# Kernel tuning notes

Hardware: AMD Instinct MI355X
Metric: run time of the kernel (lower is better)

## Reference

```python
import jax, jax.numpy as jnp
import numpy as np

# dims
B, T, D, H, DFF, NTYPE = 8, 1024, 512, 8, 1024, 341
HD = D // H                    # 64 head dim
NUM_AXES = 1
DPR = D // H // (NUM_AXES + 1) # 32 dims rotated per axis
EPS = 1e-5
THETA = 10000.0


def layernorm(x, g, b):
    m = jnp.mean(x, axis=-1, keepdims=True)
    v = jnp.mean((x - m) ** 2, axis=-1, keepdims=True)
    return (x - m) * jax.lax.rsqrt(v + EPS) * g + b


def swiglu(x):
    a, gate = jnp.split(x, 2, axis=-1)
    return jax.nn.silu(gate) * a


def apply_rope(x, pos):
    # x: [B,H,T,DPR], pos: [B,T] float positions (possibly non-integer / scrambled order)
    inv_freq = 1.0 / (THETA ** (jnp.arange(0, DPR, 2, dtype=jnp.float32) / DPR))  # [DPR/2]
    freqs = pos[:, None, :, None] * inv_freq          # [B,1,T,DPR/2]
    cos = jnp.repeat(jnp.cos(freqs), 2, axis=-1)      # each freq repeated twice -> [B,1,T,DPR]
    sin = jnp.repeat(jnp.sin(freqs), 2, axis=-1)
    x1 = x[..., 0::2]
    x2 = x[..., 1::2]
    rot = jnp.stack([-x2, x1], axis=-1).reshape(x.shape)  # rotate_half, interleaved pairs
    return x * cos + rot * sin


def setup_inputs() -> dict:
    key = jax.random.key(0)
    ks = jax.random.split(key, 16)
    s = lambda d: 1.0 / np.sqrt(d)
    return {
        "x_type": jax.random.randint(ks[0], (B, T + 1), 0, NTYPE),
        "x_value": jax.random.normal(ks[1], (B, T, D), dtype=jnp.float32),
        "seq_order": jax.random.uniform(ks[2], (B, T + 1), dtype=jnp.float32) * T,
        "W_attn": jax.random.normal(ks[3], (D, 3 * D), dtype=jnp.float32) * s(D),
        "type_emb": jax.random.normal(ks[4], (NTYPE, 2 * D), dtype=jnp.float32) * 0.02,
        "ln1_g": jnp.ones((D,), jnp.float32),
        "ln1_b": jnp.zeros((D,), jnp.float32),
        "ln2_g": jnp.ones((D,), jnp.float32),
        "ln2_b": jnp.zeros((D,), jnp.float32),
        "W1": jax.random.normal(ks[5], (D, 2 * DFF), dtype=jnp.float32) * s(D),
        "b1": jnp.zeros((2 * DFF,), jnp.float32),
        "W2": jax.random.normal(ks[6], (DFF, D), dtype=jnp.float32) * s(DFF),
        "b2": jnp.zeros((D,), jnp.float32),
    }


def reference(x_type, x_value, seq_order, W_attn, type_emb, ln1_g, ln1_b, ln2_g, ln2_b, W1, b1, W2, b2):
    # --- attention sublayer ---
    h = layernorm(x_value, ln1_g, ln1_b)                  # [B,T,D]
    qkv = h @ W_attn                                      # [B,T,3D]
    q, k, v = jnp.split(qkv, 3, axis=-1)
    emb = type_emb[x_type]                                # [B,T+1,2D]
    q_embed, k_embed = jnp.split(emb, 2, axis=-1)
    q = q + q_embed[:, :-1]
    k = k + k_embed[:, 1:]
    # [B,H,T,HD]
    to_heads = lambda t: t.reshape(B, T, H, HD).transpose(0, 2, 1, 3)
    q, k, v = to_heads(q), to_heads(k), to_heads(v)
    # rotate first DPR dims with (shifted) seq_order; remaining dims untouched
    q = jnp.concatenate([apply_rope(q[..., :DPR], seq_order[:, :-1]), q[..., DPR:]], axis=-1)
    k = jnp.concatenate([apply_rope(k[..., :DPR], seq_order[:, 1:]), k[..., DPR:]], axis=-1)
    # causal SDPA
    scores = jnp.einsum("bhqd,bhkd->bhqk", q, k) / jnp.sqrt(jnp.float32(HD))
    causal = jnp.tril(jnp.ones((T, T), dtype=bool))
    scores = jnp.where(causal, scores, -jnp.inf)
    attn = jax.nn.softmax(scores, axis=-1)
    out = jnp.einsum("bhqk,bhkd->bhqd", attn, v)          # [B,H,T,HD]
    out = out.transpose(0, 2, 1, 3).reshape(B, T, D)
    x = x_value + out
    # --- SwiGLU FFN sublayer ---
    h2 = layernorm(x, ln2_g, ln2_b)
    ff = swiglu(h2 @ W1 + b1) @ W2 + b2
    return x + ff
```

## Files before the change

kernel.cpp:

```cpp
#include <hip/hip_runtime.h>
#include <stdint.h>
#include <math.h>

typedef unsigned short u16;
typedef unsigned int u32;
typedef __attribute__((ext_vector_type(8))) short bf16x8;
typedef __attribute__((ext_vector_type(4))) float f32x4;
typedef __attribute__((ext_vector_type(2))) float f32x2;
typedef __attribute__((ext_vector_type(2))) u16 u16x2;
typedef __attribute__((ext_vector_type(8))) u16 u16x8;
typedef __attribute__((ext_vector_type(2))) u32 u32x2;

#define B_ 8
#define T_ 1024
#define D_ 512
#define H_ 8
#define TP1 1025
#define QSCALE 0.1803368801111204f

__device__ __forceinline__ u16 f2b(float f) {
  union { float f; u32 u; } v; v.f = f;
  return (u16)((v.u + 0x7fffu + ((v.u >> 16) & 1u)) >> 16);
}
__device__ __forceinline__ void gld16(const void* g, void* l) {
  __builtin_amdgcn_global_load_lds((const __attribute__((address_space(1))) u32*)g,
                                   (__attribute__((address_space(3))) u32*)l, 16, 0, 0);
}
__device__ __forceinline__ f32x4 mfma16(bf16x8 a, bf16x8 b, f32x4 c) {
  return __builtin_amdgcn_mfma_f32_16x16x32_bf16(a, b, c, 0, 0, 0);
}
__device__ __forceinline__ u32 cvtpk(float lo, float hi) {
  u32 r;
  asm("v_cvt_pk_bf16_f32 %0, %1, %2" : "=v"(r) : "v"(lo), "v"(hi));
  return r;
}
union U8 { u32 u[4]; bf16x8 v; };

#define WAITV(N) asm volatile("s_waitcnt vmcnt(" #N ")" ::: "memory")

__global__ __launch_bounds__(256) void prep_kernel(const float* __restrict__ W_attn,
    const float* __restrict__ W1, const float* __restrict__ W2,
    const float* __restrict__ seq,
    u16* __restrict__ WtA, u16* __restrict__ W1i, u16* __restrict__ W2t,
    float* __restrict__ cq, float* __restrict__ sq_,
    float* __restrict__ ck, float* __restrict__ sk) {
  int bid = blockIdx.x, tid = threadIdx.x;
  if (bid >= 576) {
    int i = (bid - 576) * 256 + tid;
    int p = i & 15, bt = i >> 4, b = bt >> 10, t = bt & 1023;
    float inv = expf(-(float)p * 0.5756462732485115f);
    float aq = seq[b * TP1 + t] * inv;
    float ak = seq[b * TP1 + t + 1] * inv;
    cq[i] = cosf(aq); sq_[i] = sinf(aq);
    ck[i] = cosf(ak); sk[i] = sinf(ak);
    return;
  }
  __shared__ u16 lt[64][65];
  const float* src; u16* dst; int ld, Kd, k0, r0; bool ilv = false;
  if (bid < 192) {
    src = W_attn; dst = WtA; ld = 1536; Kd = 512;
    k0 = (bid & 7) * 64; r0 = (bid >> 3) * 64;
  } else if (bid < 448) {
    int t = bid - 192;
    src = W1; dst = W1i; ld = 2048; Kd = 512; ilv = true;
    k0 = (t & 7) * 64; r0 = (t >> 3) * 64;
  } else {
    int t = bid - 448;
    src = W2; dst = W2t; ld = 512; Kd = 1024;
    k0 = (t & 15) * 64; r0 = (t >> 4) * 64;
  }
  int nl = tid & 63;
  int scol, rloc;
  if (ilv) {
    if (nl < 32) { scol = (r0 >> 1) + nl;          rloc = ((nl >> 4) << 5) + (nl & 15); }
    else         { scol = 1024 + (r0 >> 1) + (nl - 32); rloc = (((nl - 32) >> 4) << 5) + 16 + (nl & 15); }
  } else { scol = r0 + nl; rloc = nl; }
  #pragma unroll
  for (int it = 0; it < 16; it++) {
    int kl = (tid >> 6) * 16 + it;
    lt[rloc][kl] = f2b(src[(size_t)(k0 + kl) * ld + scol]);
  }
  __syncthreads();
  #pragma unroll
  for (int it = 0; it < 16; it++) {
    int rl = (tid >> 6) * 16 + it;
    dst[(size_t)(r0 + rl) * Kd + k0 + nl] = lt[rl][nl];
  }
}

__global__ __launch_bounds__(256) void ln_kernel(const float* __restrict__ x,
    const float* __restrict__ g, const float* __restrict__ bta, u16* __restrict__ out) {
  int row = blockIdx.x * 4 + (threadIdx.x >> 6);
  int lane = threadIdx.x & 63;
  const float* xr = x + (size_t)row * D_ + lane * 8;
  f32x4 v0 = *(const f32x4*)xr;
  f32x4 v1 = *(const f32x4*)(xr + 4);
  float s = 0.f, sq = 0.f;
  #pragma unroll
  for (int j = 0; j < 4; j++) { s += v0[j] + v1[j]; sq += v0[j] * v0[j] + v1[j] * v1[j]; }
  #pragma unroll
  for (int m = 1; m < 64; m <<= 1) { s += __shfl_xor(s, m); sq += __shfl_xor(sq, m); }
  float mean = s * (1.f / D_);
  float var = sq * (1.f / D_) - mean * mean;
  float rstd = rsqrtf(var + 1e-5f);
  f32x4 g0 = *(const f32x4*)(g + lane * 8);
  f32x4 g1 = *(const f32x4*)(g + lane * 8 + 4);
  f32x4 b0 = *(const f32x4*)(bta + lane * 8);
  f32x4 b1 = *(const f32x4*)(bta + lane * 8 + 4);
  u16x8 o;
  #pragma unroll
  for (int j = 0; j < 4; j++) {
    o[j]     = f2b((v0[j] - mean) * rstd * g0[j] + b0[j]);
    o[4 + j] = f2b((v1[j] - mean) * rstd * g1[j] + b1[j]);
  }
  *(u16x8*)(out + (size_t)row * D_ + lane * 8) = o;
}

__global__ __launch_bounds__(256) void gemm_qkv(const u16* __restrict__ A,
    const u16* __restrict__ Bt,
    const int* __restrict__ x_type, const float* __restrict__ type_emb,
    const float* __restrict__ rqc, const float* __restrict__ rqs,
    const float* __restrict__ rkc, const float* __restrict__ rks,
    u16* __restrict__ qT, u16* __restrict__ kT, u16* __restrict__ vT) {
  __shared__ u16 lA[3][4096];
  __shared__ u16 lB[3][4096];
  const int K = 512, NK = 16;
  const int tid = threadIdx.x, lane = tid & 63, w = tid >> 6;
  const int wm = w >> 1, wn = w & 1;
  int swz = (blockIdx.x & 7) * 96 + (blockIdx.x >> 3);
  int byy = swz / 12, bxx = swz - byy * 12;
  const size_t bm = (size_t)byy * 128;
  const size_t bn = (size_t)bxx * 128;

  const int r0 = tid >> 2;
  const int cs = ((tid & 3) ^ ((r0 >> 1) & 3)) * 8;
  const u16* a0 = A + (bm + r0) * K + cs;
  const u16* a1 = A + (bm + 64 + r0) * K + cs;
  const u16* b0 = Bt + (bn + r0) * K + cs;
  const u16* b1p = Bt + (bn + 64 + r0) * K + cs;

  int aoff[4], boff[4];
  #pragma unroll
  for (int i = 0; i < 4; i++) {
    int ra = wm * 64 + i * 16 + (lane & 15);
    aoff[i] = ra * 64 + (((lane >> 4) ^ ((ra >> 1) & 3)) * 16);
    int rb = wn * 64 + i * 16 + (lane & 15);
    boff[i] = rb * 64 + (((lane >> 4) ^ ((rb >> 1) & 3)) * 16);
  }

  auto stage = [&](int j, int buf) {
    char* ad = (char*)lA + buf * 8192 + w * 1024;
    char* bd = (char*)lB + buf * 8192 + w * 1024;
    gld16(a0 + j * 32, ad);
    gld16(a1 + j * 32, ad + 4096);
    gld16(b0 + j * 32, bd);
    gld16(b1p + j * 32, bd + 4096);
  };
  f32x4 acc[4][4] = {};
  auto compute = [&](int buf) {
    const char* lAc = (const char*)lA + buf * 8192;
    const char* lBc = (const char*)lB + buf * 8192;
    bf16x8 af[4], bf[4];
    #pragma unroll
    for (int i = 0; i < 4; i++) af[i] = *(const bf16x8*)(lAc + aoff[i]);
    #pragma unroll
    for (int n = 0; n < 4; n++) bf[n] = *(const bf16x8*)(lBc + boff[n]);
    __builtin_amdgcn_s_setprio(1);
    #pragma unroll
    for (int i = 0; i < 4; i++)
      #pragma unroll
      for (int n = 0; n < 4; n++)
        acc[i][n] = mfma16(af[i], bf[n], acc[i][n]);
    __builtin_amdgcn_s_setprio(0);
  };

  stage(0, 0);
  stage(1, 1);
  int cur = 0;
  for (int j = 0; j < NK - 1; j++) {
    WAITV(4);
    __builtin_amdgcn_s_barrier();
    if (j + 2 < NK) { int nb = cur + 2; if (nb >= 3) nb -= 3; stage(j + 2, nb); }
    compute(cur);
    cur = (cur + 1 == 3) ? 0 : cur + 1;
  }
  WAITV(0);
  __builtin_amdgcn_s_barrier();
  compute(cur);

  const int region = (int)(bn >> 9);
  #pragma unroll
  for (int i = 0; i < 4; i++) {
    #pragma unroll
    for (int jj = 0; jj < 4; jj++) {
      int row = (int)bm + wm * 64 + i * 16 + (lane >> 4) * 4 + jj;
      int b = row >> 10, t = row & 1023;
      if (region == 0) {
        int ty = x_type[b * TP1 + t];
        #pragma unroll
        for (int n = 0; n < 4; n++) {
          int cloc = (int)bn + wn * 64 + n * 16 + (lane & 15);
          int h = cloc >> 6, hd = cloc & 63;
          float v = acc[i][n][jj] + type_emb[(size_t)ty * 1024 + cloc];
          float vp = __shfl_xor(v, 1);
          if (hd < 32) {
            int p = hd >> 1;
            float c = rqc[row * 16 + p], s = rqs[row * 16 + p];
            v = (hd & 1) ? (v * c + vp * s) : (v * c - vp * s);
          }
          qT[((size_t)(b * 8 + h) * T_ + t) * 64 + hd] = f2b(v * QSCALE);
        }
      } else if (region == 1) {
        int ty = x_type[b * TP1 + t + 1];
        #pragma unroll
        for (int n = 0; n < 4; n++) {
          int cloc = (int)bn - 512 + wn * 64 + n * 16 + (lane & 15);
          int h = cloc >> 6, hd = cloc & 63;
          float v = acc[i][n][jj] + type_emb[(size_t)ty * 1024 + 512 + cloc];
          float vp = __shfl_xor(v, 1);
          if (hd < 32) {
            int p = hd >> 1;
            float c = rkc[row * 16 + p], s = rks[row * 16 + p];
            v = (hd & 1) ? (v * c + vp * s) : (v * c - vp * s);
          }
          kT[((size_t)(b * 8 + h) * T_ + t) * 64 + hd] = f2b(v);
        }
      } else {
        #pragma unroll
        for (int n = 0; n < 4; n++) {
          int cloc = (int)bn - 1024 + wn * 64 + n * 16 + (lane & 15);
          int h = cloc >> 6, hd = cloc & 63;
          vT[((size_t)(b * 8 + h) * 64 + hd) * T_ + t] = f2b(acc[i][n][jj]);
        }
      }
    }
  }
}

__global__ __launch_bounds__(256) void gemm_ff1(const u16* __restrict__ A,
    const u16* __restrict__ Bt, const float* __restrict__ b1,
    u16* __restrict__ outp) {
  __shared__ u16 lA[3][4096];
  __shared__ u16 lB[3][4096];
  const int K = 512, NK = 16;
  const int tid = threadIdx.x, lane = tid & 63, w = tid >> 6;
  const int wm = w >> 1, wn = w & 1;
  int swz = (blockIdx.x & 7) * 128 + (blockIdx.x >> 3);
  int byy = swz >> 4, bxx = swz & 15;
  const size_t bm = (size_t)byy * 128;
  const size_t bn = (size_t)bxx * 128;

  const int r0 = tid >> 2;
  const int cs = ((tid & 3) ^ ((r0 >> 1) & 3)) * 8;
  const u16* a0 = A + (bm + r0) * K + cs;
  const u16* a1 = A + (bm + 64 + r0) * K + cs;
  const u16* b0 = Bt + (bn + r0) * K + cs;
  const u16* b1p = Bt + (bn + 64 + r0) * K + cs;

  int aoff[4], boff[4];
  #pragma unroll
  for (int i = 0; i < 4; i++) {
    int ra = wm * 64 + i * 16 + (lane & 15);
    aoff[i] = ra * 64 + (((lane >> 4) ^ ((ra >> 1) & 3)) * 16);
    int rb = wn * 64 + i * 16 + (lane & 15);
    boff[i] = rb * 64 + (((lane >> 4) ^ ((rb >> 1) & 3)) * 16);
  }

  auto stage = [&](int j, int buf) {
    char* ad = (char*)lA + buf * 8192 + w * 1024;
    char* bd = (char*)lB + buf * 8192 + w * 1024;
    gld16(a0 + j * 32, ad);
    gld16(a1 + j * 32, ad + 4096);
    gld16(b0 + j * 32, bd);
    gld16(b1p + j * 32, bd + 4096);
  };
  f32x4 acc[4][4] = {};
  auto compute = [&](int buf) {
    const char* lAc = (const char*)lA + buf * 8192;
    const char* lBc = (const char*)lB + buf * 8192;
    bf16x8 af[4], bf[4];
    #pragma unroll
    for (int i = 0; i < 4; i++) af[i] = *(const bf16x8*)(lAc + aoff[i]);
    #pragma unroll
    for (int n = 0; n < 4; n++) bf[n] = *(const bf16x8*)(lBc + boff[n]);
    __builtin_amdgcn_s_setprio(1);
    #pragma unroll
    for (int i = 0; i < 4; i++)
      #pragma unroll
      for (int n = 0; n < 4; n++)
        acc[i][n] = mfma16(af[i], bf[n], acc[i][n]);
    __builtin_amdgcn_s_setprio(0);
  };

  stage(0, 0);
  stage(1, 1);
  int cur = 0;
  for (int j = 0; j < NK - 1; j++) {
    WAITV(4);
    __builtin_amdgcn_s_barrier();
    if (j + 2 < NK) { int nb = cur + 2; if (nb >= 3) nb -= 3; stage(j + 2, nb); }
    compute(cur);
    cur = (cur + 1 == 3) ? 0 : cur + 1;
  }
  WAITV(0);
  __builtin_amdgcn_s_barrier();
  compute(cur);

  #pragma unroll
  for (int np = 0; np < 2; np++) {
    int c = ((int)bn >> 1) + wn * 32 + np * 16 + (lane & 15);
    float bav = b1[c], bgv = b1[1024 + c];
    #pragma unroll
    for (int i = 0; i < 4; i++) {
      #pragma unroll
      for (int jj = 0; jj < 4; jj++) {
        int row = (int)bm + wm * 64 + i * 16 + (lane >> 4) * 4 + jj;
        float av = acc[i][2 * np][jj] + bav;
        float gv = acc[i][2 * np + 1][jj] + bgv;
        float sg = gv / (1.f + expf(-gv));
        outp[(size_t)row * 1024 + c] = f2b(sg * av);
      }
    }
  }
}

__global__ __launch_bounds__(512) void gemm_ff2(const u16* __restrict__ A,
    const u16* __restrict__ Bt, const float* __restrict__ bias,
    float* __restrict__ C) {
  __shared__ u16 lA[3][4096];
  __shared__ u16 lB[3][4096];
  const int K = 1024, N = 512, NK = 32;
  const int tid = threadIdx.x, lane = tid & 63, w = tid >> 6;
  const int wm = w >> 2, wn = w & 3;
  int swz = (blockIdx.x & 7) * 32 + (blockIdx.x >> 3);
  int byy = swz >> 2, bxx = swz & 3;
  const size_t bm = (size_t)byy * 128;
  const size_t bn = (size_t)bxx * 128;

  const int r0 = tid >> 2;
  const int cs = ((tid & 3) ^ ((r0 >> 1) & 3)) * 8;
  const u16* a0 = A + (bm + r0) * K + cs;
  const u16* b0 = Bt + (bn + r0) * K + cs;

  int aoff[4], boff[2];
  #pragma unroll
  for (int i = 0; i < 4; i++) {
    int ra = wm * 64 + i * 16 + (lane & 15);
    aoff[i] = ra * 64 + (((lane >> 4) ^ ((ra >> 1) & 3)) * 16);
  }
  #pragma unroll
  for (int n = 0; n < 2; n++) {
    int rb = wn * 32 + n * 16 + (lane & 15);
    boff[n] = rb * 64 + (((lane >> 4) ^ ((rb >> 1) & 3)) * 16);
  }

  auto stage = [&](int j, int buf) {
    gld16(a0 + j * 32, (char*)lA + buf * 8192 + w * 1024);
    gld16(b0 + j * 32, (char*)lB + buf * 8192 + w * 1024);
  };
  f32x4 acc[4][2] = {};
  auto compute = [&](int buf) {
    const char* lAc = (const char*)lA + buf * 8192;
    const char* lBc = (const char*)lB + buf * 8192;
    bf16x8 af[4], bf[2];
    #pragma unroll
    for (int i = 0; i < 4; i++) af[i] = *(const bf16x8*)(lAc + aoff[i]);
    #pragma unroll
    for (int n = 0; n < 2; n++) bf[n] = *(const bf16x8*)(lBc + boff[n]);
    __builtin_amdgcn_s_setprio(1);
    #pragma unroll
    for (int i = 0; i < 4; i++)
      #pragma unroll
      for (int n = 0; n < 2; n++)
        acc[i][n] = mfma16(af[i], bf[n], acc[i][n]);
    __builtin_amdgcn_s_setprio(0);
  };

  stage(0, 0);
  stage(1, 1);
  int cur = 0;
  for (int j = 0; j < NK - 1; j++) {
    WAITV(2);
    __builtin_amdgcn_s_barrier();
    if (j + 2 < NK) { int nb = cur + 2; if (nb >= 3) nb -= 3; stage(j + 2, nb); }
    compute(cur);
    cur = (cur + 1 == 3) ? 0 : cur + 1;
  }
  WAITV(0);
  __builtin_amdgcn_s_barrier();
  compute(cur);

  #pragma unroll
  for (int i = 0; i < 4; i++) {
    size_t mrow = bm + wm * 64 + i * 16 + (lane >> 4) * 4;
    #pragma unroll
    for (int n = 0; n < 2; n++) {
      size_t col = bn + wn * 32 + n * 16 + (lane & 15);
      float bv = bias[col];
      #pragma unroll
      for (int jj = 0; jj < 4; jj++) {
        size_t idx = (mrow + jj) * (size_t)N + col;
        C[idx] = acc[i][n][jj] + bv + C[idx];
      }
    }
  }
}

__global__ __launch_bounds__(512, 4) void attn_kernel(const u16* __restrict__ qT,
    const u16* __restrict__ kT, const u16* __restrict__ vT,
    const float* __restrict__ xv, float* __restrict__ X) {
  int s0 = (blockIdx.x & 7) * 64 + (blockIdx.x >> 3);
  const int xcd = blockIdx.x & 7;
  (void)xcd;
  const int bh = ((blockIdx.x & 7) << 3) + (s0 & 7);
  const int qp = 7 - ((s0 >> 3) & 7);
  const int b = bh >> 3, h = bh & 7;
  const int tid = threadIdx.x, lane = tid & 63, w = tid >> 6;
  const int q = lane & 15, g = lane >> 4;
  __shared__ u16 lK[2][8192];
  __shared__ u16 lV[2][8192];

  const int qrow0 = qp * 128 + w * 16;
  bf16x8 qf[2];
  {
    const u16* qp_ = qT + ((size_t)bh * T_ + qrow0 + q) * 64 + g * 8;
    qf[0] = *(const bf16x8*)qp_;
    qf[1] = *(const bf16x8*)(qp_ + 32);
  }
  f32x4 acc[4] = {};
  float mr = -1e30f, lr = 0.f;

  const int sr = tid >> 3;
  const int scs = ((tid & 7) ^ (sr & 7)) * 8;
  const u16* kb = kT + ((size_t)bh * T_ + sr) * 64 + scs;
  const u16* vb = vT + ((size_t)bh * 64 + sr) * T_ + scs;

  auto stage = [&](int j, int buf) {
    char* kd = (char*)lK + buf * 16384 + w * 1024;
    char* vd = (char*)lV + buf * 16384 + w * 1024;
    gld16(kb + (size_t)j * 8192, kd);
    gld16(kb + (size_t)j * 8192 + 4096, kd + 8192);
    gld16(vb + j * 128, vd);
    gld16(vb + j * 128 + 64, vd + 8192);
  };

  const int jmax = qp + 1;
  stage(0, 0);
  __syncthreads();
  int cur = 0;
  for (int j = 0; j < jmax; j++) {
    if (j + 1 < jmax) stage(j + 1, cur ^ 1);
    const char* lKc = (const char*)lK + cur * 16384;
    const char* lVc = (const char*)lV + cur * 16384;

    f32x4 s[8] = {};
    __builtin_amdgcn_s_setprio(1);
    #pragma unroll
    for (int ka = 0; ka < 2; ka++) {
      #pragma unroll
      for (int n = 0; n < 8; n++) {
        bf16x8 kf = *(const bf16x8*)(lKc + (n >> 2) * 8192 + ((n & 3) * 16 + q) * 128 +
                                     (((ka * 4 + g) ^ (q & 7)) * 16));
        s[n] = mfma16(kf, qf[ka], s[n]);
      }
    }
    __builtin_amdgcn_s_setprio(0);
    if (j == jmax - 1) {
      int qrow = w * 16 + q;
      #pragma unroll
      for (int n = 0; n < 8; n++)
        #pragma unroll
        for (int i = 0; i < 4; i++)
          if (n * 16 + g * 4 + i > qrow) s[n][i] = -1e30f;
    }
    float mt = -1e30f;
    #pragma unroll
    for (int n = 0; n < 8; n++)
      mt = fmaxf(mt, fmaxf(fmaxf(s[n][0], s[n][1]), fmaxf(s[n][2], s[n][3])));
    mt = fmaxf(mt, __shfl_xor(mt, 16));
    mt = fmaxf(mt, __shfl_xor(mt, 32));
    if (__any(mt > mr + 8.f)) {
      float mnew = fmaxf(mr, mt);
      float sc = exp2f(mr - mnew);
      mr = mnew;
      lr *= sc;
      #pragma unroll
      for (int t = 0; t < 4; t++) acc[t] *= sc;
    }
    float ps = 0.f;
    U8 pa[4];
    #pragma unroll
    for (int kt = 0; kt < 4; kt++) {
      float p0[4], p1[4];
      #pragma unroll
      for (int i = 0; i < 4; i++) {
        p0[i] = exp2f(s[2 * kt][i] - mr);
        p1[i] = exp2f(s[2 * kt + 1][i] - mr);
        ps += p0[i] + p1[i];
      }
      pa[kt].u[0] = cvtpk(p0[0], p0[1]);
      pa[kt].u[1] = cvtpk(p0[2], p0[3]);
      pa[kt].u[2] = cvtpk(p1[0], p1[1]);
      pa[kt].u[3] = cvtpk(p1[2], p1[3]);
    }
    ps += __shfl_xor(ps, 16);
    ps += __shfl_xor(ps, 32);
    lr += ps;
    __builtin_amdgcn_s_setprio(1);
    #pragma unroll
    for (int t = 0; t < 4; t++) {
      #pragma unroll
      for (int kt = 0; kt < 4; kt++) {
        const char* vrh = lVc + (kt >> 1) * 8192 + (t * 16 + q) * 128 + (g & 1) * 8;
        int ktl = kt & 1;
        u32x2 lo = *(const u32x2*)(vrh + (((ktl * 4 + (g >> 1)) ^ (q & 7)) * 16));
        u32x2 hi = *(const u32x2*)(vrh + (((ktl * 4 + 2 + (g >> 1)) ^ (q & 7)) * 16));
        U8 af;
        af.u[0] = lo[0]; af.u[1] = lo[1]; af.u[2] = hi[0]; af.u[3] = hi[1];
        acc[t] = mfma16(af.v, pa[kt].v, acc[t]);
      }
    }
    __builtin_amdgcn_s_setprio(0);
    __syncthreads();
    cur ^= 1;
  }
  {
    float inv = 1.f / lr;
    size_t base = ((size_t)b * T_ + qrow0 + q) * D_ + h * 64 + g * 4;
    #pragma unroll
    for (int t = 0; t < 4; t++) {
      f32x4 r = *(const f32x4*)(xv + base + t * 16);
      f32x4 o;
      #pragma unroll
      for (int i = 0; i < 4; i++) o[i] = r[i] + acc[t][i] * inv;
      *(f32x4*)(X + base + t * 16) = o;
    }
  }
}

extern "C" void kernel_launch(void* const* d_in, const int* in_sizes, int n_in,
                              void* d_out, int out_size, void* d_ws, size_t ws_size,
                              hipStream_t stream) {
  const int*   x_type   = (const int*)d_in[0];
  const float* x_value  = (const float*)d_in[1];
  const float* seq      = (const float*)d_in[2];
  const float* W_attn   = (const float*)d_in[3];
  const float* type_emb = (const float*)d_in[4];
  const float* ln1_g    = (const float*)d_in[5];
  const float* ln1_b    = (const float*)d_in[6];
  const float* ln2_g    = (const float*)d_in[7];
  const float* ln2_b    = (const float*)d_in[8];
  const float* W1       = (const float*)d_in[9];
  const float* b1       = (const float*)d_in[10];
  const float* W2       = (const float*)d_in[11];
  const float* b2       = (const float*)d_in[12];
  float* out = (float*)d_out;
  char* ws = (char*)d_ws;

  u16*   WtA  = (u16*)(ws + 0);
  u16*   W1i  = (u16*)(ws + 1572864);
  u16*   W2t  = (u16*)(ws + 3670016);
  float* rqc  = (float*)(ws + 4718592);
  float* rqs  = (float*)(ws + 5242880);
  float* rkc  = (float*)(ws + 5767168);
  float* rks  = (float*)(ws + 6291456);
  u16*   hbuf = (u16*)(ws + 6815744);
  u16*   qTb  = (u16*)(ws + 15204352);
  u16*   kTb  = (u16*)(ws + 23592960);
  u16*   vTb  = (u16*)(ws + 31981568);
  u16*   ff1a = (u16*)(ws + 15204352);

  prep_kernel<<<1088, 256, 0, stream>>>(W_attn, W1, W2, seq, WtA, W1i, W2t,
                                        rqc, rqs, rkc, rks);
  ln_kernel<<<B_ * T_ / 4, 256, 0, stream>>>(x_value, ln1_g, ln1_b, hbuf);
  gemm_qkv<<<768, 256, 0, stream>>>(hbuf, WtA, x_type, type_emb,
                                    rqc, rqs, rkc, rks, qTb, kTb, vTb);
  attn_kernel<<<512, 512, 0, stream>>>(qTb, kTb, vTb, x_value, out);
  ln_kernel<<<B_ * T_ / 4, 256, 0, stream>>>(out, ln2_g, ln2_b, hbuf);
  gemm_ff1<<<1024, 256, 0, stream>>>(hbuf, W1i, b1, ff1a);
  gemm_ff2<<<256, 512, 0, stream>>>(ff1a, W2t, b2, out);
}
```

Measured before the change: 134.0 us.

## Retile FF1 GEMM to 256x128 blocks with 8 waves and double buffering

The FF1 GEMM moves from 128x128 tiles with 4 waves and a 3-stage async pipeline to 256x128 tiles with 8 waves (2x4) and a 2-buffer loop synchronised by __syncthreads. Each wave now computes 128x32 and loads A fragments one at a time inside the MFMA loop. The larger tile is meant to improve reuse of B and halve the block count. In exchange it drops the deeper prefetch and the fine-grained vmcnt waits, which can expose load latency and barrier stalls. Unused xcd variables are also removed from the attention kernel.

Measured after the change: 131.7 us. Within noise of the previous version (-1.7%).

```diff
diff --git a/kernel.cpp b/kernel.cpp
--- a/kernel.cpp
+++ b/kernel.cpp
@@ -237,86 +237,77 @@
   }
 }
 
-__global__ __launch_bounds__(256) void gemm_ff1(const u16* __restrict__ A,
+__global__ __launch_bounds__(512) void gemm_ff1(const u16* __restrict__ A,
     const u16* __restrict__ Bt, const float* __restrict__ b1,
     u16* __restrict__ outp) {
-  __shared__ u16 lA[3][4096];
-  __shared__ u16 lB[3][4096];
-  const int K = 512, NK = 16;
+  __shared__ u16 lA[2][8192];
+  __shared__ u16 lB[2][4096];
+  const int K = 512;
   const int tid = threadIdx.x, lane = tid & 63, w = tid >> 6;
-  const int wm = w >> 1, wn = w & 1;
-  int swz = (blockIdx.x & 7) * 128 + (blockIdx.x >> 3);
+  const int wm = w >> 2, wn = w & 3;
+  int swz = (blockIdx.x & 7) * 64 + (blockIdx.x >> 3);
   int byy = swz >> 4, bxx = swz & 15;
-  const size_t bm = (size_t)byy * 128;
+  const size_t bm = (size_t)byy * 256;
   const size_t bn = (size_t)bxx * 128;
 
   const int r0 = tid >> 2;
   const int cs = ((tid & 3) ^ ((r0 >> 1) & 3)) * 8;
   const u16* a0 = A + (bm + r0) * K + cs;
-  const u16* a1 = A + (bm + 64 + r0) * K + cs;
+  const u16* a1 = A + (bm + 128 + r0) * K + cs;
   const u16* b0 = Bt + (bn + r0) * K + cs;
-  const u16* b1p = Bt + (bn + 64 + r0) * K + cs;
-
-  int aoff[4], boff[4];
-  #pragma unroll
-  for (int i = 0; i < 4; i++) {
-    int ra = wm * 64 + i * 16 + (lane & 15);
+
+  int aoff[8], boff[2];
+  #pragma unroll
+  for (int i = 0; i < 8; i++) {
+    int ra = wm * 128 + i * 16 + (lane & 15);
     aoff[i] = ra * 64 + (((lane >> 4) ^ ((ra >> 1) & 3)) * 16);
-    int rb = wn * 64 + i * 16 + (lane & 15);
-    boff[i] = rb * 64 + (((lane >> 4) ^ ((rb >> 1) & 3)) * 16);
-  }
-
-  auto stage = [&](int j, int buf) {
-    char* ad = (char*)lA + buf * 8192 + w * 1024;
+  }
+  #pragma unroll
+  for (int n = 0; n < 2; n++) {
+    int rb = wn * 32 + n * 16 + (lane & 15);
+    boff[n] = rb * 64 + (((lane >> 4) ^ ((rb >> 1) & 3)) * 16);
+  }
+
+  auto stage = [&](int k0, int buf) {
+    char* ad = (char*)lA + buf * 16384 + w * 1024;
     char* bd = (char*)lB + buf * 8192 + w * 1024;
-    gld16(a0 + j * 32, ad);
-    gld16(a1 + j * 32, ad + 4096);
-    gld16(b0 + j * 32, bd);
-    gld16(b1p + j * 32, bd + 4096);
+    gld16(a0 + k0, ad);
+    gld16(a1 + k0, ad + 8192);
+    gld16(b0 + k0, bd);
   };
-  f32x4 acc[4][4] = {};
-  auto compute = [&](int buf) {
-    const char* lAc = (const char*)lA + buf * 8192;
-    const char* lBc = (const char*)lB + buf * 8192;
-    bf16x8 af[4], bf[4];
-    #pragma unroll
-    for (int i = 0; i < 4; i++) af[i] = *(const bf16x8*)(lAc + aoff[i]);
-    #pragma unroll
-    for (int n = 0; n < 4; n++) bf[n] = *(const bf16x8*)(lBc + boff[n]);
+
+  f32x4 acc[8][2] = {};
+  stage(0, 0);
+  __syncthreads();
+  int cur = 0;
+  for (int k0 = 0; k0 < K; k0 += 32) {
+    if (k0 + 32 < K) stage(k0 + 32, cur ^ 1);
+    const char* lAc = (const char*)lA + cur * 16384;
+    const char* lBc = (const char*)lB + cur * 8192;
+    bf16x8 bf[2];
+    #pragma unroll
+    for (int n = 0; n < 2; n++) bf[n] = *(const bf16x8*)(lBc + boff[n]);
     __builtin_amdgcn_s_setprio(1);
     #pragma unroll
-    for (int i = 0; i < 4; i++)
-      #pragma unroll
-      for (int n = 0; n < 4; n++)
-        acc[i][n] = mfma16(af[i], bf[n], acc[i][n]);
+    for (int i = 0; i < 8; i++) {
+      bf16x8 af = *(const bf16x8*)(lAc + aoff[i]);
+      acc[i][0] = mfma16(af, bf[0], acc[i][0]);
+      acc[i][1] = mfma16(af, bf[1], acc[i][1]);
+    }
     __builtin_amdgcn_s_setprio(0);
-  };
-
-  stage(0, 0);
-  stage(1, 1);
-  int cur = 0;
-  for (int j = 0; j < NK - 1; j++) {
-    WAITV(4);
-    __builtin_amdgcn_s_barrier();
-    if (j + 2 < NK) { int nb = cur + 2; if (nb >= 3) nb -= 3; stage(j + 2, nb); }
-    compute(cur);
-    cur = (cur + 1 == 3) ? 0 : cur + 1;
-  }
-  WAITV(0);
-  __builtin_amdgcn_s_barrier();
-  compute(cur);
-
-  #pragma unroll
-  for (int np = 0; np < 2; np++) {
-    int c = ((int)bn >> 1) + wn * 32 + np * 16 + (lane & 15);
+    __syncthreads();
+    cur ^= 1;
+  }
+  {
+    int c = ((int)bn >> 1) + wn * 16 + (lane & 15);
     float bav = b1[c], bgv = b1[1024 + c];
     #pragma unroll
-    for (int i = 0; i < 4; i++) {
+    for (int i = 0; i < 8; i++) {
       #pragma unroll
       for (int jj = 0; jj < 4; jj++) {
-        int row = (int)bm + wm * 64 + i * 16 + (lane >> 4) * 4 + jj;
-        float av = acc[i][2 * np][jj] + bav;
-        float gv = acc[i][2 * np + 1][jj] + bgv;
+        int row = (int)bm + wm * 128 + i * 16 + (lane >> 4) * 4 + jj;
+        float av = acc[i][0][jj] + bav;
+        float gv = acc[i][1][jj] + bgv;
         float sg = gv / (1.f + expf(-gv));
         outp[(size_t)row * 1024 + c] = f2b(sg * av);
       }
@@ -410,8 +401,6 @@
     const u16* __restrict__ kT, const u16* __restrict__ vT,
     const float* __restrict__ xv, float* __restrict__ X) {
   int s0 = (blockIdx.x & 7) * 64 + (blockIdx.x >> 3);
-  const int xcd = blockIdx.x & 7;
-  (void)xcd;
   const int bh = ((blockIdx.x & 7) << 3) + (s0 & 7);
   const int qp = 7 - ((s0 >> 3) & 7);
   const int b = bh >> 3, h = bh & 7;
@@ -577,6 +566,6 @@
                                     rqc, rqs, rkc, rks, qTb, kTb, vTb);
   attn_kernel<<<512, 512, 0, stream>>>(qTb, kTb, vTb, x_value, out);
   ln_kernel<<<B_ * T_ / 4, 256, 0, stream>>>(out, ln2_g, ln2_b, hbuf);
-  gemm_ff1<<<1024, 256, 0, stream>>>(hbuf, W1i, b1, ff1a);
+  gemm_ff1<<<512, 512, 0, stream>>>(hbuf, W1i, b1, ff1a);
   gemm_ff2<<<256, 512, 0, stream>>>(ff1a, W2t, b2, out);
 }
```
